# Optimization experiments

Measured on AMD Instinct MI355X. Metric: run time of the kernel, lower is better.

Reference implementation:

```python
import jax, jax.numpy as jnp
import numpy as np

H, DK, DV, D = 16, 64, 64, 1024  # num_heads, q/k size, v size, embedding_dim


def setup_inputs() -> dict:
    key = jax.random.key(0)
    k1, k2, k3, k4 = jax.random.split(key, 4)
    scale = 1.0 / np.sqrt(D)
    X = jax.random.normal(k1, (4, 2048, D), dtype=jnp.float32)
    # stacked per-head projection weights (one Linear per head in the original ModuleList)
    Wq = jax.random.normal(k2, (H, D, DK), dtype=jnp.float32) * scale
    Wk = jax.random.normal(k3, (H, D, DK), dtype=jnp.float32) * scale
    Wv = jax.random.normal(k4, (H, D, DV), dtype=jnp.float32) * scale
    return {"X": X, "Wq": Wq, "Wk": Wk, "Wv": Wv}


def reference(X, Wq, Wk, Wv):
    # Batched equivalent of looping over per-head attention layers and concatenating.
    q = jnp.einsum("bsd,hde->bhse", X, Wq)  # [B,H,S,DK]
    k = jnp.einsum("bsd,hde->bhse", X, Wk)  # [B,H,S,DK]
    v = jnp.einsum("bsd,hde->bhse", X, Wv)  # [B,H,S,DV]
    scores = jnp.einsum("bhqe,bhke->bhqk", q, k) / jnp.sqrt(jnp.asarray(DK, q.dtype))
    attn = jax.nn.softmax(scores, axis=-1)
    out = jnp.einsum("bhqk,bhke->bhqe", attn, v)  # [B,H,S,DV]
    B, _, S, _ = out.shape
    # concat over heads along last dim (head order preserved)
    return out.transpose(0, 2, 1, 3).reshape(B, S, H * DV)
```

## Files before the change

kernel.cpp:

```cpp
#include <hip/hip_runtime.h>
#include <hip/hip_bf16.h>
#include <stdint.h>

typedef __attribute__((ext_vector_type(8))) short bf16x8;
typedef __attribute__((ext_vector_type(4))) float f32x4;
typedef __attribute__((ext_vector_type(16))) float f32x16;

__device__ __forceinline__ unsigned short f2bf(float f) {
  union { float f; unsigned u; } v; v.f = f;
  unsigned r = (v.u + 0x7FFFu + ((v.u >> 16) & 1u)) >> 16;
  return (unsigned short)r;
}

__device__ __forceinline__ void gload16(const void* g, void* l) {
  __builtin_amdgcn_global_load_lds(
      (const __attribute__((address_space(1))) void*)g,
      (__attribute__((address_space(3))) void*)l, 16, 0, 0);
}

__device__ __forceinline__ bf16x8 lds_read8(const unsigned short* base, int row, int k0) {
  int byteoff = row * 128 + (((k0 >> 3) ^ (row & 7)) << 4);
  return *(const bf16x8*)((const char*)base + byteoff);
}

__device__ __forceinline__ unsigned int cvtpk(float a, float b) {
  unsigned int r;
  asm("v_cvt_pk_bf16_f32 %0, %1, %2" : "=v"(r) : "v"(a), "v"(b));
  return r;
}

__global__ void cvt_x_kernel(const float* __restrict__ X, unsigned short* __restrict__ Xb) {
  int i = blockIdx.x * blockDim.x + threadIdx.x;
  const float4* src = (const float4*)X;
  float4 a = src[2 * i];
  float4 b = src[2 * i + 1];
  bf16x8 o;
  o[0] = (short)f2bf(a.x); o[1] = (short)f2bf(a.y);
  o[2] = (short)f2bf(a.z); o[3] = (short)f2bf(a.w);
  o[4] = (short)f2bf(b.x); o[5] = (short)f2bf(b.y);
  o[6] = (short)f2bf(b.z); o[7] = (short)f2bf(b.w);
  *(bf16x8*)(Xb + (size_t)i * 8) = o;
}

__global__ void cvt_w_kernel(const float* __restrict__ Wq, const float* __restrict__ Wk,
                             const float* __restrict__ Wv, unsigned short* __restrict__ Wbt) {
  __shared__ float t[64][65];
  const int k0 = blockIdx.x * 64;
  const int h  = blockIdx.y;
  const int p  = blockIdx.z;
  const float* W = (p == 0 ? Wq : (p == 1 ? Wk : Wv)) + (size_t)h * 1024 * 64;
  const int tid = threadIdx.x;
  {
    int e = tid & 63, kq = tid >> 6;
#pragma unroll
    for (int i = 0; i < 16; ++i) {
      int k = i * 4 + kq;
      t[k][e] = W[(size_t)(k0 + k) * 64 + e];
    }
  }
  __syncthreads();
  {
    int k = tid & 63, eq = tid >> 6;
#pragma unroll
    for (int i = 0; i < 16; ++i) {
      int e = i * 4 + eq;
      Wbt[(size_t)((p * 1024) + h * 64 + e) * 1024 + k0 + k] = f2bf(t[k][e]);
    }
  }
}

__global__ __launch_bounds__(256, 2) void proj_gemm(
    const unsigned short* __restrict__ Xb,
    const unsigned short* __restrict__ Wbt,
    unsigned short* __restrict__ Qb,
    unsigned short* __restrict__ Kb,
    unsigned short* __restrict__ Vt) {
  __shared__ unsigned short As[128 * 64];
  __shared__ unsigned short Bs[128 * 64];
  const int m0 = blockIdx.x * 128;
  const int n0 = blockIdx.y * 128;
  const int p  = blockIdx.z;
  const int tid = threadIdx.x;
  const int lane = tid & 63;
  const int wid = tid >> 6;
  const int wr = wid >> 1, wc = wid & 1;

  const unsigned short* Ag = Xb + (size_t)m0 * 1024;
  const unsigned short* Bg = Wbt + (size_t)p * 1024 * 1024 + (size_t)n0 * 1024;

  f32x4 acc[4][4];
#pragma unroll
  for (int i = 0; i < 4; ++i)
#pragma unroll
    for (int j = 0; j < 4; ++j) acc[i][j] = (f32x4){0.f, 0.f, 0.f, 0.f};

  for (int kt = 0; kt < 16; ++kt) {
#pragma unroll
    for (int i = 0; i < 4; ++i) {
      int row0 = wid * 32 + i * 8;
      int lr = row0 + (lane >> 3);
      int slot = (lane & 7) ^ (lr & 7);
      gload16(Ag + (size_t)lr * 1024 + kt * 64 + slot * 8, (char*)As + row0 * 128);
      gload16(Bg + (size_t)lr * 1024 + kt * 64 + slot * 8, (char*)Bs + row0 * 128);
    }
    __syncthreads();
#pragma unroll
    for (int ks = 0; ks < 2; ++ks) {
      int k0 = ks * 32 + (lane >> 4) * 8;
      bf16x8 a[4], b[4];
#pragma unroll
      for (int mi = 0; mi < 4; ++mi) a[mi] = lds_read8(As, wr * 64 + mi * 16 + (lane & 15), k0);
#pragma unroll
      for (int ni = 0; ni < 4; ++ni) b[ni] = lds_read8(Bs, wc * 64 + ni * 16 + (lane & 15), k0);
#pragma unroll
      for (int mi = 0; mi < 4; ++mi)
#pragma unroll
        for (int ni = 0; ni < 4; ++ni)
          acc[mi][ni] = __builtin_amdgcn_mfma_f32_16x16x32_bf16(a[mi], b[ni], acc[mi][ni], 0, 0, 0);
    }
    __syncthreads();
  }

#pragma unroll
  for (int mi = 0; mi < 4; ++mi) {
    int m = m0 + wr * 64 + mi * 16 + ((lane >> 4) << 2);
    int bb = m >> 11;
    int s  = m & 2047;
#pragma unroll
    for (int ni = 0; ni < 4; ++ni) {
      int n = n0 + wc * 64 + ni * 16 + (lane & 15);
      int h = n >> 6, e = n & 63;
#pragma unroll
      for (int r = 0; r < 4; ++r) {
        float v = acc[mi][ni][r];
        int sr = s + r;
        if (p == 0) {
          Qb[((size_t)(bb * 16 + h) * 2048 + sr) * 64 + e] = f2bf(v * 0.18033688f);
        } else if (p == 1) {
          Kb[((size_t)(bb * 16 + h) * 2048 + sr) * 64 + e] = f2bf(v);
        } else {
          int spos = (sr & ~12) | ((sr & 4) << 1) | ((sr & 8) >> 1);
          Vt[((size_t)(bb * 16 + h) * 64 + e) * 2048 + spos] = f2bf(v);
        }
      }
    }
  }
}

__global__ __launch_bounds__(256, 4) void attn_kernel(
    const unsigned short* __restrict__ Qb,
    const unsigned short* __restrict__ Kb,
    const unsigned short* __restrict__ Vt,
    float* __restrict__ out) {
  __shared__ unsigned short smem[16384];
  const int bh = blockIdx.x;
  const int q0 = blockIdx.y * 128;
  const int tid = threadIdx.x;
  const int lane = tid & 63;
  const int wid = tid >> 6;
  const int ql = lane & 31;
  const int hi = lane >> 5;

  const unsigned short* Qp = Qb + (size_t)bh * 2048 * 64;
  const unsigned short* Kp = Kb + (size_t)bh * 2048 * 64;
  const unsigned short* Vp = Vt + (size_t)bh * 64 * 2048;

  bf16x8 qf[4];
#pragma unroll
  for (int ks = 0; ks < 4; ++ks)
    qf[ks] = *(const bf16x8*)(Qp + (size_t)(q0 + wid * 32 + ql) * 64 + ks * 16 + hi * 8);

  f32x16 acc[2];
#pragma unroll
  for (int mi = 0; mi < 2; ++mi)
#pragma unroll
    for (int i = 0; i < 16; ++i) acc[mi][i] = 0.f;
  float l = 0.f;

  auto STAGE = [&](int buf, int kt) {
    unsigned short* Ks = smem + buf * 8192;
    unsigned short* Vs = Ks + 4096;
#pragma unroll
    for (int i = 0; i < 2; ++i) {
      int row0 = wid * 16 + i * 8;
      int lr = row0 + (lane >> 3);
      int slot = (lane & 7) ^ (lr & 7);
      gload16(Kp + (size_t)(kt * 64 + lr) * 64 + slot * 8, (char*)Ks + row0 * 128);
      gload16(Vp + (size_t)lr * 2048 + kt * 64 + slot * 8, (char*)Vs + row0 * 128);
    }
  };

  STAGE(0, 0);
  asm volatile("s_waitcnt vmcnt(0)" ::: "memory");
  __builtin_amdgcn_s_barrier();

  int cur = 0;
  for (int kt = 0; kt < 32; ++kt) {
    if (kt < 31) STAGE(cur ^ 1, kt + 1);
    const unsigned short* Ks = smem + cur * 8192;
    const unsigned short* Vs = Ks + 4096;

#pragma unroll
    for (int t = 0; t < 2; ++t) {
      f32x16 s;
#pragma unroll
      for (int i = 0; i < 16; ++i) s[i] = 0.f;
#pragma unroll
      for (int ks = 0; ks < 4; ++ks) {
        bf16x8 kf = lds_read8(Ks, t * 32 + ql, ks * 16 + hi * 8);
        s = __builtin_amdgcn_mfma_f32_32x32x16_bf16(kf, qf[ks], s, 0, 0, 0);
      }

#pragma unroll
      for (int i = 0; i < 16; ++i) s[i] = exp2f(s[i]);

      {
        float sm[8];
#pragma unroll
        for (int i = 0; i < 8; ++i) sm[i] = s[i] + s[i + 8];
        float sa = (sm[0] + sm[1]) + (sm[2] + sm[3]);
        float sb = (sm[4] + sm[5]) + (sm[6] + sm[7]);
        l += sa + sb;
      }

      union { unsigned int u[4]; bf16x8 v; } P0, P1;
#pragma unroll
      for (int j = 0; j < 4; ++j) {
        P0.u[j] = cvtpk(s[2 * j],     s[2 * j + 1]);
        P1.u[j] = cvtpk(s[8 + 2 * j], s[8 + 2 * j + 1]);
      }

#pragma unroll
      for (int mi = 0; mi < 2; ++mi) {
        bf16x8 v0 = lds_read8(Vs, mi * 32 + ql, t * 32 + hi * 8);
        bf16x8 v1 = lds_read8(Vs, mi * 32 + ql, t * 32 + 16 + hi * 8);
        acc[mi] = __builtin_amdgcn_mfma_f32_32x32x16_bf16(v0, P0.v, acc[mi], 0, 0, 0);
        acc[mi] = __builtin_amdgcn_mfma_f32_32x32x16_bf16(v1, P1.v, acc[mi], 0, 0, 0);
      }
    }

    asm volatile("s_waitcnt vmcnt(0)" ::: "memory");
    __builtin_amdgcn_s_barrier();
    cur ^= 1;
  }

  __builtin_amdgcn_s_barrier();

  float lf = l + __shfl_xor(l, 32, 64);
  float inv = 1.0f / lf;
  float* fs = (float*)smem + wid * 2048;
#pragma unroll
  for (int mi = 0; mi < 2; ++mi)
#pragma unroll
    for (int r = 0; r < 16; ++r) {
      int e = mi * 32 + (r & 3) + 8 * (r >> 2) + 4 * hi;
      fs[ql * 64 + (e ^ ql)] = acc[mi][r] * inv;
    }
  const int b = bh >> 4, h = bh & 15;
#pragma unroll
  for (int i = 0; i < 32; ++i) {
    float v = fs[i * 64 + (lane ^ i)];
    out[((size_t)(b * 2048 + q0 + wid * 32 + i)) * 1024 + h * 64 + lane] = v;
  }
}

extern "C" void kernel_launch(void* const* d_in, const int* in_sizes, int n_in,
                              void* d_out, int out_size, void* d_ws, size_t ws_size,
                              hipStream_t stream) {
  (void)in_sizes; (void)n_in; (void)out_size; (void)ws_size;
  const float* X  = (const float*)d_in[0];
  const float* Wq = (const float*)d_in[1];
  const float* Wk = (const float*)d_in[2];
  const float* Wv = (const float*)d_in[3];
  float* out = (float*)d_out;

  unsigned short* Xb  = (unsigned short*)d_ws;
  unsigned short* Wbt = Xb + (size_t)8192 * 1024;
  unsigned short* Qb  = Wbt + (size_t)3 * 1024 * 1024;
  unsigned short* Kb  = Qb + (size_t)64 * 2048 * 64;
  unsigned short* Vt  = Kb + (size_t)64 * 2048 * 64;

  hipLaunchKernelGGL(cvt_x_kernel, dim3(4096), dim3(256), 0, stream, X, Xb);
  hipLaunchKernelGGL(cvt_w_kernel, dim3(16, 16, 3), dim3(256), 0, stream, Wq, Wk, Wv, Wbt);
  hipLaunchKernelGGL(proj_gemm, dim3(64, 8, 3), dim3(256), 0, stream, Xb, Wbt, Qb, Kb, Vt);
  hipLaunchKernelGGL(attn_kernel, dim3(64, 16), dim3(256), 0, stream, Qb, Kb, Vt, out);
}
```

Measured before the change: 177.5 us.

## Process two 32-row query tiles per wave to reuse K/V LDS fragments

Each wave now computes attention for 64 query rows instead of 32, so every K and V fragment read from LDS feeds two MFMA chains. The block's query tile doubles to 256, the grid halves along the query dimension, and the launch-bounds occupancy target drops from 4 to 2 blocks. LDS addresses are precomputed once per lane and combined with XOR offsets, replacing per-read swizzle arithmetic. The intent is to halve LDS reads and global K/V traffic per query. The cost is more registers per thread, lower occupancy, and fewer blocks to spread across the GPU's compute units.

```diff
diff --git a/kernel.cpp b/kernel.cpp
--- a/kernel.cpp
+++ b/kernel.cpp
@@ -21,6 +21,10 @@
 __device__ __forceinline__ bf16x8 lds_read8(const unsigned short* base, int row, int k0) {
   int byteoff = row * 128 + (((k0 >> 3) ^ (row & 7)) << 4);
   return *(const bf16x8*)((const char*)base + byteoff);
+}
+
+__device__ __forceinline__ bf16x8 lds_at(const unsigned short* smem, unsigned off) {
+  return *(const bf16x8*)((const char*)smem + off);
 }
 
 __device__ __forceinline__ unsigned int cvtpk(float a, float b) {
@@ -147,14 +151,14 @@
   }
 }
 
-__global__ __launch_bounds__(256, 4) void attn_kernel(
+__global__ __launch_bounds__(256, 2) void attn_kernel(
     const unsigned short* __restrict__ Qb,
     const unsigned short* __restrict__ Kb,
     const unsigned short* __restrict__ Vt,
     float* __restrict__ out) {
   __shared__ unsigned short smem[16384];
   const int bh = blockIdx.x;
-  const int q0 = blockIdx.y * 128;
+  const int q0 = blockIdx.y * 256;
   const int tid = threadIdx.x;
   const int lane = tid & 63;
   const int wid = tid >> 6;
@@ -165,17 +169,19 @@
   const unsigned short* Kp = Kb + (size_t)bh * 2048 * 64;
   const unsigned short* Vp = Vt + (size_t)bh * 64 * 2048;
 
-  bf16x8 qf[4];
-#pragma unroll
-  for (int ks = 0; ks < 4; ++ks)
-    qf[ks] = *(const bf16x8*)(Qp + (size_t)(q0 + wid * 32 + ql) * 64 + ks * 16 + hi * 8);
-
-  f32x16 acc[2];
-#pragma unroll
-  for (int mi = 0; mi < 2; ++mi)
-#pragma unroll
-    for (int i = 0; i < 16; ++i) acc[mi][i] = 0.f;
-  float l = 0.f;
+  bf16x8 qf0[4], qf1[4];
+#pragma unroll
+  for (int ks = 0; ks < 4; ++ks) {
+    qf0[ks] = *(const bf16x8*)(Qp + (size_t)(q0 + wid * 64 + ql) * 64 + ks * 16 + hi * 8);
+    qf1[ks] = *(const bf16x8*)(Qp + (size_t)(q0 + wid * 64 + 32 + ql) * 64 + ks * 16 + hi * 8);
+  }
+
+  f32x16 a00, a01, a10, a11;
+#pragma unroll
+  for (int i = 0; i < 16; ++i) { a00[i] = 0.f; a01[i] = 0.f; a10[i] = 0.f; a11[i] = 0.f; }
+  float l0 = 0.f, l1 = 0.f;
+
+  const unsigned lane_off = (unsigned)(ql * 128 + (((ql & 7) ^ hi) << 4));
 
   auto STAGE = [&](int buf, int kt) {
     unsigned short* Ks = smem + buf * 8192;
@@ -197,46 +203,57 @@
   int cur = 0;
   for (int kt = 0; kt < 32; ++kt) {
     if (kt < 31) STAGE(cur ^ 1, kt + 1);
-    const unsigned short* Ks = smem + cur * 8192;
-    const unsigned short* Vs = Ks + 4096;
+    const unsigned cb = (unsigned)cur << 14;
 
 #pragma unroll
     for (int t = 0; t < 2; ++t) {
-      f32x16 s;
-#pragma unroll
-      for (int i = 0; i < 16; ++i) s[i] = 0.f;
+      bf16x8 kf[4];
+#pragma unroll
+      for (int ks = 0; ks < 4; ++ks)
+        kf[ks] = lds_at(smem, lane_off ^ (cb | (t << 12) | (ks << 5)));
+
+      f32x16 s0, s1;
+#pragma unroll
+      for (int i = 0; i < 16; ++i) { s0[i] = 0.f; s1[i] = 0.f; }
 #pragma unroll
       for (int ks = 0; ks < 4; ++ks) {
-        bf16x8 kf = lds_read8(Ks, t * 32 + ql, ks * 16 + hi * 8);
-        s = __builtin_amdgcn_mfma_f32_32x32x16_bf16(kf, qf[ks], s, 0, 0, 0);
+        s0 = __builtin_amdgcn_mfma_f32_32x32x16_bf16(kf[ks], qf0[ks], s0, 0, 0, 0);
+        s1 = __builtin_amdgcn_mfma_f32_32x32x16_bf16(kf[ks], qf1[ks], s1, 0, 0, 0);
       }
 
 #pragma unroll
-      for (int i = 0; i < 16; ++i) s[i] = exp2f(s[i]);
+      for (int i = 0; i < 16; ++i) { s0[i] = exp2f(s0[i]); s1[i] = exp2f(s1[i]); }
 
       {
-        float sm[8];
-#pragma unroll
-        for (int i = 0; i < 8; ++i) sm[i] = s[i] + s[i + 8];
-        float sa = (sm[0] + sm[1]) + (sm[2] + sm[3]);
-        float sb = (sm[4] + sm[5]) + (sm[6] + sm[7]);
-        l += sa + sb;
+        float sm0[8], sm1[8];
+#pragma unroll
+        for (int i = 0; i < 8; ++i) { sm0[i] = s0[i] + s0[i + 8]; sm1[i] = s1[i] + s1[i + 8]; }
+        l0 += ((sm0[0] + sm0[1]) + (sm0[2] + sm0[3])) + ((sm0[4] + sm0[5]) + (sm0[6] + sm0[7]));
+        l1 += ((sm1[0] + sm1[1]) + (sm1[2] + sm1[3])) + ((sm1[4] + sm1[5]) + (sm1[6] + sm1[7]));
       }
 
-      union { unsigned int u[4]; bf16x8 v; } P0, P1;
+      union { unsigned int u[4]; bf16x8 v; } P00, P01, P10, P11;
 #pragma unroll
       for (int j = 0; j < 4; ++j) {
-        P0.u[j] = cvtpk(s[2 * j],     s[2 * j + 1]);
-        P1.u[j] = cvtpk(s[8 + 2 * j], s[8 + 2 * j + 1]);
+        P00.u[j] = cvtpk(s0[2 * j],     s0[2 * j + 1]);
+        P01.u[j] = cvtpk(s0[8 + 2 * j], s0[8 + 2 * j + 1]);
+        P10.u[j] = cvtpk(s1[2 * j],     s1[2 * j + 1]);
+        P11.u[j] = cvtpk(s1[8 + 2 * j], s1[8 + 2 * j + 1]);
       }
 
-#pragma unroll
-      for (int mi = 0; mi < 2; ++mi) {
-        bf16x8 v0 = lds_read8(Vs, mi * 32 + ql, t * 32 + hi * 8);
-        bf16x8 v1 = lds_read8(Vs, mi * 32 + ql, t * 32 + 16 + hi * 8);
-        acc[mi] = __builtin_amdgcn_mfma_f32_32x32x16_bf16(v0, P0.v, acc[mi], 0, 0, 0);
-        acc[mi] = __builtin_amdgcn_mfma_f32_32x32x16_bf16(v1, P1.v, acc[mi], 0, 0, 0);
-      }
+      bf16x8 vf00 = lds_at(smem, lane_off ^ (cb | 8192u | (0 << 12) | (t << 6) | (0 << 5)));
+      bf16x8 vf01 = lds_at(smem, lane_off ^ (cb | 8192u | (0 << 12) | (t << 6) | (1 << 5)));
+      bf16x8 vf10 = lds_at(smem, lane_off ^ (cb | 8192u | (1 << 12) | (t << 6) | (0 << 5)));
+      bf16x8 vf11 = lds_at(smem, lane_off ^ (cb | 8192u | (1 << 12) | (t << 6) | (1 << 5)));
+
+      a00 = __builtin_amdgcn_mfma_f32_32x32x16_bf16(vf00, P00.v, a00, 0, 0, 0);
+      a10 = __builtin_amdgcn_mfma_f32_32x32x16_bf16(vf00, P10.v, a10, 0, 0, 0);
+      a00 = __builtin_amdgcn_mfma_f32_32x32x16_bf16(vf01, P01.v, a00, 0, 0, 0);
+      a10 = __builtin_amdgcn_mfma_f32_32x32x16_bf16(vf01, P11.v, a10, 0, 0, 0);
+      a01 = __builtin_amdgcn_mfma_f32_32x32x16_bf16(vf10, P00.v, a01, 0, 0, 0);
+      a11 = __builtin_amdgcn_mfma_f32_32x32x16_bf16(vf10, P10.v, a11, 0, 0, 0);
+      a01 = __builtin_amdgcn_mfma_f32_32x32x16_bf16(vf11, P01.v, a01, 0, 0, 0);
+      a11 = __builtin_amdgcn_mfma_f32_32x32x16_bf16(vf11, P11.v, a11, 0, 0, 0);
     }
 
     asm volatile("s_waitcnt vmcnt(0)" ::: "memory");
@@ -246,21 +263,28 @@
 
   __builtin_amdgcn_s_barrier();
 
-  float lf = l + __shfl_xor(l, 32, 64);
-  float inv = 1.0f / lf;
+  const int b = bh >> 4, h = bh & 15;
   float* fs = (float*)smem + wid * 2048;
-#pragma unroll
-  for (int mi = 0; mi < 2; ++mi)
+
+#pragma unroll
+  for (int g = 0; g < 2; ++g) {
+    float lg = g ? l1 : l0;
+    float lf = lg + __shfl_xor(lg, 32, 64);
+    float inv = 1.0f / lf;
+    const f32x16& m0v = g ? a10 : a00;
+    const f32x16& m1v = g ? a11 : a01;
 #pragma unroll
     for (int r = 0; r < 16; ++r) {
-      int e = mi * 32 + (r & 3) + 8 * (r >> 2) + 4 * hi;
-      fs[ql * 64 + (e ^ ql)] = acc[mi][r] * inv;
-    }
-  const int b = bh >> 4, h = bh & 15;
-#pragma unroll
-  for (int i = 0; i < 32; ++i) {
-    float v = fs[i * 64 + (lane ^ i)];
-    out[((size_t)(b * 2048 + q0 + wid * 32 + i)) * 1024 + h * 64 + lane] = v;
+      int e0 = (r & 3) + 8 * (r >> 2) + 4 * hi;
+      fs[ql * 64 + (e0 ^ ql)] = m0v[r] * inv;
+      int e1 = 32 + e0;
+      fs[ql * 64 + (e1 ^ ql)] = m1v[r] * inv;
+    }
+#pragma unroll
+    for (int i = 0; i < 32; ++i) {
+      float v = fs[i * 64 + (lane ^ i)];
+      out[((size_t)(b * 2048 + q0 + wid * 64 + g * 32 + i)) * 1024 + h * 64 + lane] = v;
+    }
   }
 }
 
@@ -283,5 +307,5 @@
   hipLaunchKernelGGL(cvt_x_kernel, dim3(4096), dim3(256), 0, stream, X, Xb);
   hipLaunchKernelGGL(cvt_w_kernel, dim3(16, 16, 3), dim3(256), 0, stream, Wq, Wk, Wv, Wbt);
   hipLaunchKernelGGL(proj_gemm, dim3(64, 8, 3), dim3(256), 0, stream, Xb, Wbt, Qb, Kb, Vt);
-  hipLaunchKernelGGL(attn_kernel, dim3(64, 16), dim3(256), 0, stream, Qb, Kb, Vt, out);
-}
+  hipLaunchKernelGGL(attn_kernel, dim3(64, 8), dim3(256), 0, stream, Qb, Kb, Vt, out);
+}
```

Result: faster. 171.8 us (-3.2%).
